# Kernel optimization log

Measured on AMD Instinct MI355X. Metric: run time of the kernel, lower is better.

Reference implementation:

```python
import jax, jax.numpy as jnp
import numpy as np

B, H, W = 8, 384, 384
KH = KW = 3
STRIDE, PAD = 1, 1


def setup_inputs() -> dict:
    key = jax.random.key(0)
    ks = jax.random.split(key, 5)
    pf = jax.random.normal(ks[0], (B, 3, H, W), jnp.float32)
    cf = jax.random.normal(ks[1], (B, 3, H, W), jnp.float32)
    mv = jax.random.normal(ks[2], (B, 2, H, W), jnp.float32)
    offset_w = jax.random.normal(ks[3], (18, 8, KH, KW), jnp.float32) * 0.05
    offset_b = jnp.zeros((18,), jnp.float32)
    deform_w = jax.random.normal(ks[4], (3, 3, KH, KW), jnp.float32) * 0.1
    return dict(pf=pf, cf=cf, mv=mv, offset_w=offset_w, offset_b=offset_b, deform_w=deform_w)


def _conv2d(x, w, b):
    y = jax.lax.conv_general_dilated(
        x, w, window_strides=(STRIDE, STRIDE),
        padding=((PAD, PAD), (PAD, PAD)),
        dimension_numbers=('NCHW', 'OIHW', 'NCHW'))
    return y + b[None, :, None, None]


def _deform_conv2d(x, offset, w):
    # x: [B, Cin, H, W]; offset: [B, 2*KH*KW, Ho, Wo] (torchvision order: per tap k -> (dy, dx))
    Bn, Cin, Hn, Wn = x.shape
    Ho, Wo = offset.shape[2], offset.shape[3]
    K = KH * KW
    off = offset.reshape(Bn, K, 2, Ho, Wo)
    ky = jnp.repeat(jnp.arange(KH), KW).astype(x.dtype)   # [K] kernel row offset
    kx = jnp.tile(jnp.arange(KW), KH).astype(x.dtype)     # [K] kernel col offset
    base_y = (jnp.arange(Ho) * STRIDE - PAD).astype(x.dtype)
    base_x = (jnp.arange(Wo) * STRIDE - PAD).astype(x.dtype)
    # sampling positions p = p0 + p_k + delta_p_k, shape [B, K, Ho, Wo]
    py = off[:, :, 0] + ky[None, :, None, None] + base_y[None, None, :, None]
    px = off[:, :, 1] + kx[None, :, None, None] + base_x[None, None, None, :]
    y0 = jnp.floor(py)
    x0 = jnp.floor(px)
    wy = py - y0  # bilinear weights, [B, K, Ho, Wo]
    wx = px - x0

    def gather(yi, xi):
        # zero padding outside the image (torchvision semantics)
        valid = (yi >= 0) & (yi < Hn) & (xi >= 0) & (xi < Wn)
        yc = jnp.clip(yi, 0, Hn - 1).astype(jnp.int32)
        xc = jnp.clip(xi, 0, Wn - 1).astype(jnp.int32)
        v = jax.vmap(lambda im, y, xg: im[:, y, xg])(x, yc, xc)  # [B, Cin, K, Ho, Wo]
        return v * valid[:, None].astype(x.dtype)

    v00 = gather(y0, x0)
    v01 = gather(y0, x0 + 1)
    v10 = gather(y0 + 1, x0)
    v11 = gather(y0 + 1, x0 + 1)
    wy_ = wy[:, None]  # broadcast over channel dim
    wx_ = wx[:, None]
    samp = (v00 * (1 - wy_) * (1 - wx_) + v01 * (1 - wy_) * wx_
            + v10 * wy_ * (1 - wx_) + v11 * wy_ * wx_)  # [B, Cin, K, Ho, Wo]
    # weighted accumulation over taps and input channels (no bias)
    return jnp.einsum('oik,bikhw->bohw', w.reshape(w.shape[0], w.shape[1], K), samp)


def reference(pf, cf, mv, offset_w, offset_b, deform_w):
    x = jnp.concatenate([pf, cf, mv], axis=1)          # [B, 8, H, W]
    offset = _conv2d(x, offset_w, offset_b)            # [B, 18, H, W]
    return _deform_conv2d(pf, offset, deform_w)        # [B, 3, H, W]
```

## Files before the change

kernel.cpp:

```cpp
#include <hip/hip_runtime.h>


#define Bn 8
#define Hn 384
#define Wn 384
#define HWn (Hn * Wn)
#define TILE 16
#define PH 6
#define PT 28

#define OFF_PTILE 0
#define SZ_PTILE (PT * PT * 4)
#define OFF_T8   SZ_PTILE
#define SZ_T8U   4864
#define SMEM_FLOATS (OFF_T8 + SZ_T8U)

typedef float f32x4 __attribute__((ext_vector_type(4)));
typedef short s16x8 __attribute__((ext_vector_type(8)));

__device__ inline unsigned short rne_bf16(float f) {
    unsigned u = __float_as_uint(f);
    u += 0x7fffu + ((u >> 16) & 1u);
    return (unsigned short)(u >> 16);
}

__global__ void prep_bw(const float* __restrict__ ow, unsigned short* __restrict__ bwg) {
    const int idx = blockIdx.x * 64 + threadIdx.x;
    const int sg   = idx >> 6;
    const int lane = idx & 63;
    const int s  = sg >> 1;
    const int nt = sg & 1;
    const int am = lane & 15;
    const int g  = lane >> 4;
    const int oc = nt * 16 + am;
    const int t  = 4 * s + g;
    union { unsigned short h[8]; s16x8 v; } F;
#pragma unroll
    for (int c = 0; c < 8; ++c) {
        float w = 0.f;
        if (t < 9 && oc < 18) w = ow[oc * 72 + c * 9 + t];
        F.h[c] = rne_bf16(w);
    }
    ((s16x8*)bwg)[idx] = F.v;
}

__global__ __launch_bounds__(256, 5) void guided_cnn_fused(
    const float* __restrict__ pf, const float* __restrict__ cf,
    const float* __restrict__ mv, const s16x8* __restrict__ bwg,
    const float* __restrict__ ob, const float* __restrict__ dw,
    float* __restrict__ out)
{
    __shared__ float smem[SMEM_FLOATS];

    const int tid = threadIdx.x;
    const int b = blockIdx.z;
    const int tileY0 = blockIdx.y * TILE;
    const int tileX0 = blockIdx.x * TILE;
    const int oy = tileY0 - PH;
    const int ox = tileX0 - PH;

    float* ptile4 = smem + OFF_PTILE;
    float* t8b    = smem + OFF_T8;

    const int lane = tid & 63;
    const int wv   = tid >> 6;
    const int am   = lane & 15;
    const int g    = lane >> 4;

    s16x8 bfrag[3][2];
#pragma unroll
    for (int s = 0; s < 3; ++s)
#pragma unroll
        for (int nt = 0; nt < 2; ++nt)
            bfrag[s][nt] = bwg[(s * 2 + nt) * 64 + lane];

    for (int p = tid; p < PT * PT; p += 256) {
        const int row = p / PT;
        const int col = p - row * PT;
        const int gy = oy + row, gx = ox + col;
        const bool v = ((unsigned)gy < (unsigned)Hn) && ((unsigned)gx < (unsigned)Wn);
        const size_t gidx = (size_t)b * 3 * HWn + gy * Wn + gx;
        f32x4 q;
        q[0] = v ? pf[gidx] : 0.f;
        q[1] = v ? pf[gidx + HWn] : 0.f;
        q[2] = v ? pf[gidx + 2 * HWn] : 0.f;
        q[3] = 0.f;
        *(f32x4*)(ptile4 + p * 4) = q;
    }
    for (int p = tid; p < 324; p += 256) {
        const int row = p / 18;
        const int col = p - row * 18;
        const int gy = tileY0 + row - 1, gx = tileX0 + col - 1;
        const bool v = ((unsigned)gy < (unsigned)Hn) && ((unsigned)gx < (unsigned)Wn);
        const size_t base = (size_t)b * 3 * HWn + gy * Wn + gx;
        float c0 = v ? pf[base] : 0.f;
        float c1 = v ? pf[base + HWn] : 0.f;
        float c2 = v ? pf[base + 2 * HWn] : 0.f;
        float c3 = v ? cf[base] : 0.f;
        float c4 = v ? cf[base + HWn] : 0.f;
        float c5 = v ? cf[base + 2 * HWn] : 0.f;
        const size_t mbase = (size_t)b * 2 * HWn + gy * Wn + gx;
        float c6 = v ? mv[mbase] : 0.f;
        float c7 = v ? mv[mbase + HWn] : 0.f;
        union { unsigned u[4]; f32x4 f; } P;
        P.u[0] = (unsigned)rne_bf16(c0) | ((unsigned)rne_bf16(c1) << 16);
        P.u[1] = (unsigned)rne_bf16(c2) | ((unsigned)rne_bf16(c3) << 16);
        P.u[2] = (unsigned)rne_bf16(c4) | ((unsigned)rne_bf16(c5) << 16);
        P.u[3] = (unsigned)rne_bf16(c6) | ((unsigned)rne_bf16(c7) << 16);
        *(f32x4*)(t8b + p * 4) = P.f;
    }
    __syncthreads();

    f32x4 acc[4][2];
#pragma unroll
    for (int mt = 0; mt < 4; ++mt)
#pragma unroll
        for (int nt = 0; nt < 2; ++nt)
            acc[mt][nt] = (f32x4){0.f, 0.f, 0.f, 0.f};

#pragma unroll
    for (int mt = 0; mt < 4; ++mt) {
        const int mrow = wv * 4 + mt;
#pragma unroll
        for (int s = 0; s < 3; ++s) {
            const int tap = 4 * s + g;
            const int tc  = tap < 9 ? tap : 8;
            const int dy = tc / 3, dx = tc - dy * 3;
            union { f32x4 f; s16x8 v; } A;
            A.f = *(const f32x4*)(t8b + ((mrow + dy) * 18 + (am + dx)) * 4);
            acc[mt][0] = __builtin_amdgcn_mfma_f32_16x16x32_bf16(A.v, bfrag[s][0], acc[mt][0], 0, 0, 0);
            acc[mt][1] = __builtin_amdgcn_mfma_f32_16x16x32_bf16(A.v, bfrag[s][1], acc[mt][1], 0, 0, 0);
        }
    }
    __syncthreads();

    float* offb = smem + OFF_T8;
#pragma unroll
    for (int mt = 0; mt < 4; ++mt) {
        const int prow = wv * 4 + mt;
#pragma unroll
        for (int r = 0; r < 4; ++r) {
            const int pix = prow * 16 + (g * 4 + r);
            offb[pix * 19 + am] = acc[mt][0][r];
            if (am < 2) offb[pix * 19 + 16 + am] = acc[mt][1][r];
        }
    }
    __syncthreads();

    const int tx = tid & 15;
    const int ty = tid >> 4;
    const int x = tileX0 + tx;
    const int y = tileY0 + ty;

    float offs[18];
#pragma unroll
    for (int j = 0; j < 18; ++j) offs[j] = offb[tid * 19 + j] + ob[j];

    const float* p0 = pf + (size_t)b * 3 * HWn;
    float acc2[3] = {0.f, 0.f, 0.f};

#pragma unroll
    for (int k = 0; k < 9; ++k) {
        const int ky = k / 3;
        const int kx = k - ky * 3;
        const float rpy = offs[2 * k]     + (float)(ty + ky - 1 + PH);
        const float rpx = offs[2 * k + 1] + (float)(tx + kx - 1 + PH);
        const float y0f = floorf(rpy);
        const float x0f = floorf(rpx);
        const float wy = rpy - y0f;
        const float wx = rpx - x0f;
        const int ty0 = (int)y0f;
        const int tx0 = (int)x0f;
        const float w00 = (1.f - wy) * (1.f - wx);
        const float w01 = (1.f - wy) * wx;
        const float w10 = wy * (1.f - wx);
        const float w11 = wy * wx;

        const bool inT = ((unsigned)ty0 < (unsigned)(PT - 1)) &&
                         ((unsigned)tx0 < (unsigned)(PT - 1));
        if (inT) {
            const float* base = ptile4 + (ty0 * PT + tx0) * 4;
            const f32x4 q00 = *(const f32x4*)(base);
            const f32x4 q01 = *(const f32x4*)(base + 4);
            const f32x4 q10 = *(const f32x4*)(base + 4 * PT);
            const f32x4 q11 = *(const f32x4*)(base + 4 * PT + 4);
#pragma unroll
            for (int i = 0; i < 3; ++i) {
                const float s = w00 * q00[i] + w01 * q01[i] + w10 * q10[i] + w11 * q11[i];
#pragma unroll
                for (int o = 0; o < 3; ++o)
                    acc2[o] = fmaf(dw[o * 27 + i * 9 + k], s, acc2[o]);
            }
        } else {
            const int y0 = ty0 + oy, x0 = tx0 + ox;
            const int y1 = y0 + 1,  x1 = x0 + 1;
            const bool vy0 = ((unsigned)y0 < (unsigned)Hn);
            const bool vy1 = ((unsigned)y1 < (unsigned)Hn);
            const bool vx0 = ((unsigned)x0 < (unsigned)Wn);
            const bool vx1 = ((unsigned)x1 < (unsigned)Wn);
            const int y0c = min(max(y0, 0), Hn - 1);
            const int y1c = min(max(y1, 0), Hn - 1);
            const int x0c = min(max(x0, 0), Wn - 1);
            const int x1c = min(max(x1, 0), Wn - 1);
            const int i00 = y0c * Wn + x0c;
            const int i01 = y0c * Wn + x1c;
            const int i10 = y1c * Wn + x0c;
            const int i11 = y1c * Wn + x1c;
#pragma unroll
            for (int i = 0; i < 3; ++i) {
                const float* pl = p0 + (size_t)i * HWn;
                const float v00 = (vy0 && vx0) ? pl[i00] : 0.f;
                const float v01 = (vy0 && vx1) ? pl[i01] : 0.f;
                const float v10 = (vy1 && vx0) ? pl[i10] : 0.f;
                const float v11 = (vy1 && vx1) ? pl[i11] : 0.f;
                const float s = w00 * v00 + w01 * v01 + w10 * v10 + w11 * v11;
#pragma unroll
                for (int o = 0; o < 3; ++o)
                    acc2[o] = fmaf(dw[o * 27 + i * 9 + k], s, acc2[o]);
            }
        }
    }

#pragma unroll
    for (int o = 0; o < 3; ++o) {
        out[(((size_t)b * 3 + o) * Hn + y) * Wn + x] = acc2[o];
    }
}

extern "C" void kernel_launch(void* const* d_in, const int* in_sizes, int n_in,
                              void* d_out, int out_size, void* d_ws, size_t ws_size,
                              hipStream_t stream) {
    const float* pf = (const float*)d_in[0];
    const float* cf = (const float*)d_in[1];
    const float* mv = (const float*)d_in[2];
    const float* ow = (const float*)d_in[3];
    const float* ob = (const float*)d_in[4];
    const float* dw = (const float*)d_in[5];
    float* out = (float*)d_out;
    unsigned short* bwg = (unsigned short*)d_ws;

    prep_bw<<<6, 64, 0, stream>>>(ow, bwg);
    dim3 grid(Wn / TILE, Hn / TILE, Bn);
    guided_cnn_fused<<<grid, 256, 0, stream>>>(pf, cf, mv, (const s16x8*)bwg, ob, dw, out);
}
```

Baseline: 118.6 us.

## Shrink pf halo tile, pack to 3 channels, vectorize bilinear with packed FMA

Cuts the pf shared tile halo from 6 to 4 pixels and stores 3 floats per pixel instead of 4, which shrinks shared memory, and raises the launch-bounds occupancy hint from 5 to 6. The offset bias now initializes the MFMA accumulators instead of being added per thread later. The bilinear interpolation and output accumulation use 2-wide float vectors for packed FMA, plus a lerp form that needs fewer multiplies. The smaller halo sends more samples with large offsets to the slower global-memory fallback path. Unaligned 3-float shared loads may also cost more than the old 16-byte loads.

```diff
diff --git a/kernel.cpp b/kernel.cpp
--- a/kernel.cpp
+++ b/kernel.cpp
@@ -6,17 +6,36 @@
 #define Wn 384
 #define HWn (Hn * Wn)
 #define TILE 16
-#define PH 6
-#define PT 28
+#define PH 4
+#define PT 24
 
 #define OFF_PTILE 0
-#define SZ_PTILE (PT * PT * 4)
+#define SZ_PTILE (PT * PT * 3)
 #define OFF_T8   SZ_PTILE
 #define SZ_T8U   4864
 #define SMEM_FLOATS (OFF_T8 + SZ_T8U)
 
 typedef float f32x4 __attribute__((ext_vector_type(4)));
+typedef float f32x2 __attribute__((ext_vector_type(2)));
 typedef short s16x8 __attribute__((ext_vector_type(8)));
+
+static __device__ inline f32x2 vfma2(f32x2 a, f32x2 b, f32x2 c) {
+#if __has_builtin(__builtin_elementwise_fma)
+    return __builtin_elementwise_fma(a, b, c);
+#else
+    f32x2 r; r.x = fmaf(a.x, b.x, c.x); r.y = fmaf(a.y, b.y, c.y); return r;
+#endif
+}
+static __device__ inline f32x2 vfloor2(f32x2 a) {
+#if __has_builtin(__builtin_elementwise_floor)
+    return __builtin_elementwise_floor(a);
+#else
+    f32x2 r; r.x = floorf(a.x); r.y = floorf(a.y); return r;
+#endif
+}
+static __device__ inline f32x2 splat2(float s) {
+    f32x2 r; r.x = s; r.y = s; return r;
+}
 
 __device__ inline unsigned short rne_bf16(float f) {
     unsigned u = __float_as_uint(f);
@@ -44,7 +63,7 @@
     ((s16x8*)bwg)[idx] = F.v;
 }
 
-__global__ __launch_bounds__(256, 5) void guided_cnn_fused(
+__global__ __launch_bounds__(256, 6) void guided_cnn_fused(
     const float* __restrict__ pf, const float* __restrict__ cf,
     const float* __restrict__ mv, const s16x8* __restrict__ bwg,
     const float* __restrict__ ob, const float* __restrict__ dw,
@@ -59,7 +78,7 @@
     const int oy = tileY0 - PH;
     const int ox = tileX0 - PH;
 
-    float* ptile4 = smem + OFF_PTILE;
+    float* ptile3 = smem + OFF_PTILE;
     float* t8b    = smem + OFF_T8;
 
     const int lane = tid & 63;
@@ -73,6 +92,9 @@
 #pragma unroll
         for (int nt = 0; nt < 2; ++nt)
             bfrag[s][nt] = bwg[(s * 2 + nt) * 64 + lane];
+
+    const float bias0 = ob[am];
+    const float bias1 = ob[am < 2 ? 16 + am : 17];
 
     for (int p = tid; p < PT * PT; p += 256) {
         const int row = p / PT;
@@ -80,12 +102,10 @@
         const int gy = oy + row, gx = ox + col;
         const bool v = ((unsigned)gy < (unsigned)Hn) && ((unsigned)gx < (unsigned)Wn);
         const size_t gidx = (size_t)b * 3 * HWn + gy * Wn + gx;
-        f32x4 q;
-        q[0] = v ? pf[gidx] : 0.f;
-        q[1] = v ? pf[gidx + HWn] : 0.f;
-        q[2] = v ? pf[gidx + 2 * HWn] : 0.f;
-        q[3] = 0.f;
-        *(f32x4*)(ptile4 + p * 4) = q;
+        float* dst = ptile3 + p * 3;
+        dst[0] = v ? pf[gidx] : 0.f;
+        dst[1] = v ? pf[gidx + HWn] : 0.f;
+        dst[2] = v ? pf[gidx + 2 * HWn] : 0.f;
     }
     for (int p = tid; p < 324; p += 256) {
         const int row = p / 18;
@@ -113,10 +133,10 @@
 
     f32x4 acc[4][2];
 #pragma unroll
-    for (int mt = 0; mt < 4; ++mt)
-#pragma unroll
-        for (int nt = 0; nt < 2; ++nt)
-            acc[mt][nt] = (f32x4){0.f, 0.f, 0.f, 0.f};
+    for (int mt = 0; mt < 4; ++mt) {
+        acc[mt][0] = (f32x4){bias0, bias0, bias0, bias0};
+        acc[mt][1] = (f32x4){bias1, bias1, bias1, bias1};
+    }
 
 #pragma unroll
     for (int mt = 0; mt < 4; ++mt) {
@@ -152,45 +172,56 @@
     const int x = tileX0 + tx;
     const int y = tileY0 + ty;
 
-    float offs[18];
-#pragma unroll
-    for (int j = 0; j < 18; ++j) offs[j] = offb[tid * 19 + j] + ob[j];
+    f32x2 offs2[9];
+#pragma unroll
+    for (int j = 0; j < 9; ++j) {
+        offs2[j].x = offb[tid * 19 + 2 * j];
+        offs2[j].y = offb[tid * 19 + 2 * j + 1];
+    }
 
     const float* p0 = pf + (size_t)b * 3 * HWn;
-    float acc2[3] = {0.f, 0.f, 0.f};
+    f32x2 accP = splat2(0.f);
+    float acc2c = 0.f;
+    const float tyf = (float)(ty + PH - 1);
+    const float txf = (float)(tx + PH - 1);
 
 #pragma unroll
     for (int k = 0; k < 9; ++k) {
         const int ky = k / 3;
         const int kx = k - ky * 3;
-        const float rpy = offs[2 * k]     + (float)(ty + ky - 1 + PH);
-        const float rpx = offs[2 * k + 1] + (float)(tx + kx - 1 + PH);
-        const float y0f = floorf(rpy);
-        const float x0f = floorf(rpx);
-        const float wy = rpy - y0f;
-        const float wx = rpx - x0f;
-        const int ty0 = (int)y0f;
-        const int tx0 = (int)x0f;
-        const float w00 = (1.f - wy) * (1.f - wx);
-        const float w01 = (1.f - wy) * wx;
-        const float w10 = wy * (1.f - wx);
-        const float w11 = wy * wx;
+        f32x2 basek;
+        basek.x = tyf + (float)ky;
+        basek.y = txf + (float)kx;
+        const f32x2 pyx = offs2[k] + basek;
+        const f32x2 fl = vfloor2(pyx);
+        const f32x2 w  = pyx - fl;
+        const int ty0 = (int)fl.x;
+        const int tx0 = (int)fl.y;
+        const float wy = w.x, wx = w.y;
 
         const bool inT = ((unsigned)ty0 < (unsigned)(PT - 1)) &&
                          ((unsigned)tx0 < (unsigned)(PT - 1));
+        float s0, s1, s2;
         if (inT) {
-            const float* base = ptile4 + (ty0 * PT + tx0) * 4;
-            const f32x4 q00 = *(const f32x4*)(base);
-            const f32x4 q01 = *(const f32x4*)(base + 4);
-            const f32x4 q10 = *(const f32x4*)(base + 4 * PT);
-            const f32x4 q11 = *(const f32x4*)(base + 4 * PT + 4);
-#pragma unroll
-            for (int i = 0; i < 3; ++i) {
-                const float s = w00 * q00[i] + w01 * q01[i] + w10 * q10[i] + w11 * q11[i];
-#pragma unroll
-                for (int o = 0; o < 3; ++o)
-                    acc2[o] = fmaf(dw[o * 27 + i * 9 + k], s, acc2[o]);
-            }
+            const float* base  = ptile3 + (ty0 * PT + tx0) * 3;
+            const float* base2 = base + 3 * PT;
+            const float a0 = base[0],  a1 = base[1],  a2 = base[2];
+            const float b0 = base[3],  b1 = base[4],  b2 = base[5];
+            const float c0 = base2[0], c1 = base2[1], c2 = base2[2];
+            const float d0 = base2[3], d1 = base2[4], d2 = base2[5];
+            f32x2 q00; q00.x = a0; q00.y = a1;
+            f32x2 q01; q01.x = b0; q01.y = b1;
+            f32x2 q10; q10.x = c0; q10.y = c1;
+            f32x2 q11; q11.x = d0; q11.y = d1;
+            const f32x2 wx2 = splat2(wx);
+            const f32x2 wy2 = splat2(wy);
+            const f32x2 h0 = vfma2(wx2, q01 - q00, q00);
+            const f32x2 h1 = vfma2(wx2, q11 - q10, q10);
+            const f32x2 s01 = vfma2(wy2, h1 - h0, h0);
+            const float h0c = fmaf(wx, b2 - a2, a2);
+            const float h1c = fmaf(wx, d2 - c2, c2);
+            s0 = s01.x; s1 = s01.y;
+            s2 = fmaf(wy, h1c - h0c, h0c);
         } else {
             const int y0 = ty0 + oy, x0 = tx0 + ox;
             const int y1 = y0 + 1,  x1 = x0 + 1;
@@ -206,6 +237,11 @@
             const int i01 = y0c * Wn + x1c;
             const int i10 = y1c * Wn + x0c;
             const int i11 = y1c * Wn + x1c;
+            const float w00 = (1.f - wy) * (1.f - wx);
+            const float w01 = (1.f - wy) * wx;
+            const float w10 = wy * (1.f - wx);
+            const float w11 = wy * wx;
+            float sv[3];
 #pragma unroll
             for (int i = 0; i < 3; ++i) {
                 const float* pl = p0 + (size_t)i * HWn;
@@ -213,18 +249,27 @@
                 const float v01 = (vy0 && vx1) ? pl[i01] : 0.f;
                 const float v10 = (vy1 && vx0) ? pl[i10] : 0.f;
                 const float v11 = (vy1 && vx1) ? pl[i11] : 0.f;
-                const float s = w00 * v00 + w01 * v01 + w10 * v10 + w11 * v11;
-#pragma unroll
-                for (int o = 0; o < 3; ++o)
-                    acc2[o] = fmaf(dw[o * 27 + i * 9 + k], s, acc2[o]);
+                sv[i] = w00 * v00 + w01 * v01 + w10 * v10 + w11 * v11;
             }
-        }
-    }
-
-#pragma unroll
-    for (int o = 0; o < 3; ++o) {
-        out[(((size_t)b * 3 + o) * Hn + y) * Wn + x] = acc2[o];
-    }
+            s0 = sv[0]; s1 = sv[1]; s2 = sv[2];
+        }
+        {
+            f32x2 dwp0; dwp0.x = dw[0 * 27 + 0 * 9 + k]; dwp0.y = dw[1 * 27 + 0 * 9 + k];
+            f32x2 dwp1; dwp1.x = dw[0 * 27 + 1 * 9 + k]; dwp1.y = dw[1 * 27 + 1 * 9 + k];
+            f32x2 dwp2; dwp2.x = dw[0 * 27 + 2 * 9 + k]; dwp2.y = dw[1 * 27 + 2 * 9 + k];
+            accP = vfma2(dwp0, splat2(s0), accP);
+            accP = vfma2(dwp1, splat2(s1), accP);
+            accP = vfma2(dwp2, splat2(s2), accP);
+            acc2c = fmaf(dw[2 * 27 + 0 * 9 + k], s0, acc2c);
+            acc2c = fmaf(dw[2 * 27 + 1 * 9 + k], s1, acc2c);
+            acc2c = fmaf(dw[2 * 27 + 2 * 9 + k], s2, acc2c);
+        }
+    }
+
+    const size_t obase = ((size_t)b * 3 * Hn + y) * Wn + x;
+    out[obase] = accP.x;
+    out[obase + HWn] = accP.y;
+    out[obase + 2 * HWn] = acc2c;
 }
 
 extern "C" void kernel_launch(void* const* d_in, const int* in_sizes, int n_in,
```

New measurement: 115.7 us. 2.4% less time.
